# Kernel tuning notes

Measured on AMD Instinct MI355X. Metric: run time of the kernel, lower is better.

Reference implementation:

```python
import jax, jax.numpy as jnp
import numpy as np

N = 50000      # nodes
E = 500000     # edges
R = 4          # num_relations
B = 512        # num graphs in batch
IN = 64        # in_embd
DIN = 6 * IN   # concat of 6 embeddings
H = 256        # layer_embd
O = 256        # out_embd
CARD = [33, 5, 3, 4, 2, 3]


def setup_inputs() -> dict:
    key = jax.random.key(0)
    ks = jax.random.split(key, 24)
    cols = [jax.random.randint(ks[i], (N,), 0, CARD[i], dtype=jnp.int32) for i in range(6)]
    x = jnp.stack(cols, axis=1)                                     # [N,6] categorical atom features
    edge_index = jax.random.randint(ks[6], (2, E), 0, N, dtype=jnp.int32)
    edge_type = jax.random.randint(ks[7], (E,), 0, R, dtype=jnp.int32)
    batch = jnp.sort(jax.random.randint(ks[8], (N,), 0, B, dtype=jnp.int32))

    def g(k, shape, scale):
        return jax.random.normal(k, shape, jnp.float32) * scale

    inp = dict(x=x, edge_index=edge_index, edge_type=edge_type, batch=batch)
    for i in range(6):
        inp[f"emb{i}"] = g(ks[9 + i], (CARD[i], IN), 1.0)
    inp["W1"] = g(ks[15], (R, DIN, H), 0.05)
    inp["root1"] = g(ks[16], (DIN, H), 0.05)
    inp["b1"] = jnp.zeros((H,), jnp.float32)
    inp["W2"] = g(ks[17], (R, H, O), 0.06)
    inp["root2"] = g(ks[18], (H, O), 0.06)
    inp["b2"] = jnp.zeros((O,), jnp.float32)
    inp["g1_w"] = g(ks[19], (O, O), 0.06)
    inp["g1_b"] = jnp.zeros((O,), jnp.float32)
    inp["bn_g"] = jnp.ones((O,), jnp.float32)
    inp["bn_b"] = jnp.zeros((O,), jnp.float32)
    inp["g2_w"] = g(ks[20], (O, 1), 0.06)
    inp["g2_b"] = jnp.zeros((1,), jnp.float32)
    inp["gl_w"] = g(ks[21], (O, 1), 0.06)
    inp["gl_b"] = jnp.zeros((1,), jnp.float32)
    return inp


def rgcn_conv(h, src, dst, etype, W, root, bias):
    # PyG RGCNConv: out_i = x_i @ root + bias + sum_r mean_{j in N_r(i)} (x_j @ W_r)
    xw = jnp.einsum('nd,rdo->rno', h, W)                 # [R,N,O] relation-transformed nodes
    msg = xw[etype, src]                                  # [E,O] gather per edge
    seg = dst * R + etype                                 # combined (node, relation) segment id
    sums = jax.ops.segment_sum(msg, seg, num_segments=N * R)
    cnt = jax.ops.segment_sum(jnp.ones((msg.shape[0],), h.dtype), seg, num_segments=N * R)
    mean = sums / jnp.maximum(cnt, 1.0)[:, None]          # per-relation mean aggregation
    agg = mean.reshape(N, R, -1).sum(axis=1)              # sum over relations
    return agg + h @ root + bias


def reference(x, edge_index, edge_type, batch,
              emb0, emb1, emb2, emb3, emb4, emb5,
              W1, root1, b1, W2, root2, b2,
              g1_w, g1_b, bn_g, bn_b, g2_w, g2_b, gl_w, gl_b):
    embs = [emb0, emb1, emb2, emb3, emb4, emb5]
    feats = jnp.concatenate([embs[i][x[:, i]] for i in range(6)], axis=1)  # [N, 6*IN]
    src, dst = edge_index[0], edge_index[1]
    h = jax.nn.sigmoid(rgcn_conv(feats, src, dst, edge_type, W1, root1, b1))
    h = jax.nn.sigmoid(rgcn_conv(h, src, dst, edge_type, W2, root2, b2))    # [N,O]

    # GlobalAttention gate_nn: Linear -> BatchNorm1d (training-mode stats) -> ReLU -> Linear
    g = h @ g1_w + g1_b
    mu = g.mean(axis=0)
    var = g.var(axis=0)                                   # biased var, as torch BN forward
    g = (g - mu) / jnp.sqrt(var + 1e-5) * bn_g + bn_b
    gate = jax.nn.relu(g) @ g2_w + g2_b                   # [N,1]

    # segment softmax over graphs
    gmax = jax.ops.segment_max(gate, batch, num_segments=B)
    e = jnp.exp(gate - gmax[batch])
    denom = jax.ops.segment_sum(e, batch, num_segments=B)
    attn = e / (denom[batch] + 1e-16)
    pooled = jax.ops.segment_sum(attn * h, batch, num_segments=B)  # [B,O]

    return jax.nn.sigmoid(pooled @ gl_w + gl_b)           # [B,1]
```

## Files before the change

kernel.cpp:

```cpp
#include <hip/hip_runtime.h>
#include <hip/hip_bf16.h>
#include <cstdint>

#define NN 50000
#define NE 500000
#define NR 4
#define NBATCH 512
#define HD 256
#define NSEG (NN*NR)

__constant__ int c_off[6] = {0,33,38,41,45,47};

__device__ __forceinline__ float sigf(float x){ return 1.0f/(1.0f+__expf(-x)); }
__device__ __forceinline__ float bf2f(unsigned short b){ return __uint_as_float((unsigned)b<<16); }
__device__ __forceinline__ unsigned short f2bf(float f){
  unsigned u = __float_as_uint(f);
  return (unsigned short)((u + 0x7fffu + ((u>>16)&1u)) >> 16);
}

typedef short bf16raw8 __attribute__((ext_vector_type(8)));
typedef float f32x4v  __attribute__((ext_vector_type(4)));
union LD16 { uint4 u; bf16raw8 v; };

__global__ void k_weff(const float* __restrict__ e0,const float* __restrict__ e1,
                       const float* __restrict__ e2,const float* __restrict__ e3,
                       const float* __restrict__ e4,const float* __restrict__ e5,
                       const float* __restrict__ W, int rstride,
                       float* __restrict__ out){
  int rc = blockIdx.x, h = threadIdx.x;
  int r = rc/50, cg = rc%50;
  int j, cl;
  if      (cg>=47){j=5;cl=cg-47;} else if (cg>=45){j=4;cl=cg-45;}
  else if (cg>=41){j=3;cl=cg-41;} else if (cg>=38){j=2;cl=cg-38;}
  else if (cg>=33){j=1;cl=cg-33;} else            {j=0;cl=cg;}
  const float* emb = j==0?e0:j==1?e1:j==2?e2:j==3?e3:j==4?e4:e5;
  const float* wb = W + (size_t)r*rstride + (size_t)(j*64)*HD + h;
  float acc = 0.f;
  #pragma unroll 8
  for (int k=0;k<64;k++) acc += emb[cl*64+k]*wb[(size_t)k*HD];
  out[(size_t)rc*HD+h] = acc;
}

__global__ void k_cnt(const int* __restrict__ ei, const int* __restrict__ et,
                      int* __restrict__ cnt){
  int e = blockIdx.x*256 + threadIdx.x;
  if (e >= NE) return;
  atomicAdd(&cnt[ei[NE+e]*NR + et[e]], 1);
}

__global__ void k_b1t(const float* __restrict__ W1eff, const float* __restrict__ R1eff,
                      unsigned short* __restrict__ B1t){
  int id = blockIdx.x*256 + threadIdx.x;
  int k = id & 255, o = id >> 8;
  float v = 0.f;
  if (k < 200) v = W1eff[(size_t)k*HD + o];
  else if (k < 250) v = R1eff[(size_t)(k-200)*HD + o];
  B1t[(size_t)o*256 + k] = f2bf(v);
}

__global__ void k_tconv(const float* __restrict__ W, unsigned short* __restrict__ Wt,
                        int K, int O){
  int id = blockIdx.x*256 + threadIdx.x;
  if (id >= K*O) return;
  int k = id % K, o = id / K;
  Wt[(size_t)o*256 + k] = f2bf(W[(size_t)k*O + o]);
}

#define SC_T 256
#define SC_NB ((NSEG/4 + SC_T - 1)/SC_T)

__global__ void k_scan1(const int* __restrict__ cnt, int* __restrict__ bsum){
  __shared__ int sh[SC_T];
  int b = blockIdx.x, t = threadIdx.x;
  int i4 = b*SC_T + t;
  int s = 0;
  if (i4 < NSEG/4){ int4 v = ((const int4*)cnt)[i4]; s = v.x+v.y+v.z+v.w; }
  sh[t] = s; __syncthreads();
  for (int o=128;o>0;o>>=1){ if (t<o) sh[t]+=sh[t+o]; __syncthreads(); }
  if (t==0) bsum[b] = sh[0];
}

__global__ void k_scan2(const int* __restrict__ bsum, int* __restrict__ boff,
                        int* __restrict__ offs){
  __shared__ int sh[256];
  int t = threadIdx.x;
  int v = (t < SC_NB) ? bsum[t] : 0;
  sh[t] = v; __syncthreads();
  for (int o=1;o<256;o<<=1){
    int add = (t>=o) ? sh[t-o] : 0; __syncthreads();
    sh[t] += add; __syncthreads();
  }
  if (t < SC_NB) boff[t] = sh[t] - v;
  if (t == 255) offs[NSEG] = sh[255];
}

__global__ void k_scan3(const int* __restrict__ cnt, const int* __restrict__ boff,
                        int* __restrict__ offs, int* __restrict__ cursor){
  __shared__ int sh[SC_T];
  int b = blockIdx.x, t = threadIdx.x;
  int i4 = b*SC_T + t;
  int4 v = {0,0,0,0};
  if (i4 < NSEG/4) v = ((const int4*)cnt)[i4];
  int s = v.x+v.y+v.z+v.w;
  sh[t] = s; __syncthreads();
  for (int o=1;o<256;o<<=1){
    int add = (t>=o) ? sh[t-o] : 0; __syncthreads();
    sh[t] += add; __syncthreads();
  }
  if (i4 < NSEG/4){
    int excl = sh[t] - s + boff[b];
    int4 ov; ov.x = excl; ov.y = ov.x+v.x; ov.z = ov.y+v.y; ov.w = ov.z+v.z;
    ((int4*)offs)[i4] = ov; ((int4*)cursor)[i4] = ov;
  }
}

__global__ void k_bin(const int* __restrict__ ei, const int* __restrict__ et,
                      int* __restrict__ cursor, int* __restrict__ esrc){
  int e = blockIdx.x*256 + threadIdx.x;
  if (e >= NE) return;
  int s = ei[e], d = ei[NE+e], t = et[e];
  int slot = atomicAdd(&cursor[d*NR + t], 1);
  esrc[slot] = s;
}

__global__ void k_buildseg(const int* __restrict__ x, const int* __restrict__ offs,
                           const int* __restrict__ esrc, unsigned short* __restrict__ A1){
  int n = blockIdx.x, t = threadIdx.x;
  float v = 0.f;
  if (t < 200){
    int r = t/50, bin = t%50;
    int j, cl;
    if      (bin>=47){j=5;cl=bin-47;} else if (bin>=45){j=4;cl=bin-45;}
    else if (bin>=41){j=3;cl=bin-41;} else if (bin>=38){j=2;cl=bin-38;}
    else if (bin>=33){j=1;cl=bin-33;} else            {j=0;cl=bin;}
    int a = offs[n*NR+r], e2 = offs[n*NR+r+1];
    int c = 0;
    for (int e=a;e<e2;e++){
      int s = esrc[e];
      c += (x[s*6+j] == cl) ? 1 : 0;
    }
    v = (float)c / (float)max(e2-a, 1);
  } else if (t < 250){
    int cg = t - 200;
    #pragma unroll
    for (int j=0;j<6;j++) if (cg == c_off[j] + x[n*6+j]) v = 1.f;
  }
  A1[(size_t)n*256 + t] = f2bf(v);
}

template<bool SIG>
__global__ __launch_bounds__(512) void k_mfma(
    const unsigned short* __restrict__ A,  int lda,
    const unsigned short* __restrict__ Bt,
    const float* __restrict__ bias,
    unsigned short* __restrict__ out0, int ldc0, int n0,
    unsigned short* __restrict__ out1, int ldc1,
    int M){
  constexpr int NK = 8;
  constexpr int K  = 256;
  int tid = threadIdx.x;
  int wave = tid >> 6, lane = tid & 63;
  int wm = (wave >> 1) * 32, wn = (wave & 1) * 64;
  int bm = blockIdx.y * 128, bn = blockIdx.x * 128;
  int lrow = lane & 15, lk8 = (lane >> 4) * 8;

  const unsigned short* aP[2];
  const unsigned short* bP[4];
  #pragma unroll
  for (int mi=0;mi<2;mi++){
    int row = bm + wm + mi*16 + lrow; if (row > M-1) row = M-1;
    aP[mi] = A + (size_t)row*lda + lk8;
  }
  #pragma unroll
  for (int nj=0;nj<4;nj++){
    int col = bn + wn + nj*16 + lrow;
    bP[nj] = Bt + (size_t)col*K + lk8;
  }

  f32x4v acc[2][4] = {};
  bf16raw8 aF[2][2], bF[2][4];

  #pragma unroll
  for (int mi=0;mi<2;mi++){ LD16 t; t.u = *(const uint4*)(aP[mi]); aF[0][mi]=t.v; }
  #pragma unroll
  for (int nj=0;nj<4;nj++){ LD16 t; t.u = *(const uint4*)(bP[nj]); bF[0][nj]=t.v; }

  #pragma unroll
  for (int k=0;k<NK;k++){
    int cur = k & 1, nxt = cur ^ 1;
    if (k+1 < NK){
      #pragma unroll
      for (int mi=0;mi<2;mi++){ LD16 t; t.u = *(const uint4*)(aP[mi] + (k+1)*32); aF[nxt][mi]=t.v; }
      #pragma unroll
      for (int nj=0;nj<4;nj++){ LD16 t; t.u = *(const uint4*)(bP[nj] + (k+1)*32); bF[nxt][nj]=t.v; }
    }
    #pragma unroll
    for (int mi=0;mi<2;mi++)
      #pragma unroll
      for (int nj=0;nj<4;nj++)
        acc[mi][nj] = __builtin_amdgcn_mfma_f32_16x16x32_bf16(aF[cur][mi], bF[cur][nj], acc[mi][nj], 0, 0, 0);
  }

  int r0 = (lane >> 4) * 4;
  #pragma unroll
  for (int mi = 0; mi < 2; mi++){
    #pragma unroll
    for (int i = 0; i < 4; i++){
      int row = bm + wm + mi*16 + r0 + i;
      if (row >= M) continue;
      #pragma unroll
      for (int nj = 0; nj < 4; nj++){
        int col = bn + wn + nj*16 + lrow;
        float v = acc[mi][nj][i];
        if (bias) v += bias[col];
        if (SIG) v = sigf(v);
        if (col < n0) out0[(size_t)row*ldc0 + col] = f2bf(v);
        else          out1[(size_t)row*ldc1 + (col - n0)] = f2bf(v);
      }
    }
  }
}

__global__ void k_comb1(const int* __restrict__ offs, const int* __restrict__ esrc,
                        const unsigned short* __restrict__ zbuf,
                        unsigned short* __restrict__ pacc){
  int gid = blockIdx.x*256 + threadIdx.x;
  int n = gid >> 6;
  if (n >= NN) return;
  int lane = gid & 63;
  float t0=0.f,t1=0.f,t2=0.f,t3=0.f;
  #pragma unroll
  for (int r=0;r<2;r++){
    int a = offs[n*NR+r], b = offs[n*NR+r+1];
    float a0=0.f,a1=0.f,a2=0.f,a3=0.f;
    for (int e=a;e<b;e++){
      int s = esrc[e];
      ushort4 v = *(const ushort4*)(zbuf + (size_t)s*512 + r*256 + lane*4);
      a0+=bf2f(v.x); a1+=bf2f(v.y); a2+=bf2f(v.z); a3+=bf2f(v.w);
    }
    float iv = 1.0f / (float)max(b-a, 1);
    t0+=a0*iv; t1+=a1*iv; t2+=a2*iv; t3+=a3*iv;
  }
  ushort4 o; o.x=f2bf(t0); o.y=f2bf(t1); o.z=f2bf(t2); o.w=f2bf(t3);
  *(ushort4*)(pacc + (size_t)n*HD + lane*4) = o;
}

__global__ void k_comb2(const int* __restrict__ offs, const int* __restrict__ esrc,
                        const unsigned short* __restrict__ zbuf,
                        const unsigned short* __restrict__ pacc,
                        const unsigned short* __restrict__ rootbuf,
                        const float* __restrict__ b2,
                        unsigned short* __restrict__ h2){
  int gid = blockIdx.x*256 + threadIdx.x;
  int n = gid >> 6;
  if (n >= NN) return;
  int lane = gid & 63;
  float t0=0.f,t1=0.f,t2=0.f,t3=0.f;
  #pragma unroll
  for (int r=0;r<2;r++){
    int a = offs[n*NR+2+r], b = offs[n*NR+2+r+1];
    float a0=0.f,a1=0.f,a2=0.f,a3=0.f;
    for (int e=a;e<b;e++){
      int s = esrc[e];
      ushort4 v = *(const ushort4*)(zbuf + (size_t)s*512 + r*256 + lane*4);
      a0+=bf2f(v.x); a1+=bf2f(v.y); a2+=bf2f(v.z); a3+=bf2f(v.w);
    }
    float iv = 1.0f / (float)max(b-a, 1);
    t0+=a0*iv; t1+=a1*iv; t2+=a2*iv; t3+=a3*iv;
  }
  ushort4 p = *(const ushort4*)(pacc + (size_t)n*HD + lane*4);
  ushort4 rt= *(const ushort4*)(rootbuf + (size_t)n*HD + lane*4);
  float4 bb = *(const float4*)(b2 + lane*4);
  ushort4 o;
  o.x = f2bf(sigf(t0 + bf2f(p.x) + bf2f(rt.x) + bb.x));
  o.y = f2bf(sigf(t1 + bf2f(p.y) + bf2f(rt.y) + bb.y));
  o.z = f2bf(sigf(t2 + bf2f(p.z) + bf2f(rt.z) + bb.z));
  o.w = f2bf(sigf(t3 + bf2f(p.w) + bf2f(rt.w) + bb.w));
  *(ushort4*)(h2 + (size_t)n*HD + lane*4) = o;
}

__global__ void k_bnstats(const unsigned short* __restrict__ g, float* __restrict__ chan){
  int c = threadIdx.x;
  int r0 = blockIdx.x*128;
  int rend = min(r0+128, NN);
  float s=0.f, q=0.f;
  for (int row=r0; row<rend; row++){
    float v = bf2f(g[(size_t)row*HD + c]);
    s += v; q += v*v;
  }
  atomicAdd(&chan[c], s); atomicAdd(&chan[HD+c], q);
}

__global__ void k_bnfin(const float* __restrict__ chan, const float* __restrict__ bng,
                        const float* __restrict__ bnb, float* __restrict__ bnp){
  int c = threadIdx.x;
  float mu = chan[c]/(float)NN;
  float var = chan[HD+c]/(float)NN - mu*mu;
  float scale = bng[c]*rsqrtf(var + 1e-5f);
  bnp[c] = bnb[c] - mu*scale;
  bnp[HD+c] = scale;
}

__global__ void k_gate(const unsigned short* __restrict__ g, const float* __restrict__ bnp,
                       const float* __restrict__ g2w, const float* __restrict__ g2b,
                       float* __restrict__ gate){
  int lane = threadIdx.x & 63;
  int n = blockIdx.x*4 + (threadIdx.x>>6);
  if (n >= NN) return;
  float s = 0.f;
  #pragma unroll
  for (int k=0;k<4;k++){
    int c = lane + k*64;
    float v = bf2f(g[(size_t)n*HD + c])*bnp[HD+c] + bnp[c];
    v = fmaxf(v, 0.f);
    s += v * g2w[c];
  }
  #pragma unroll
  for (int o=32;o>0;o>>=1) s += __shfl_down(s, o);
  if (lane==0) gate[n] = s + g2b[0];
}

__global__ void k_goffs(const int* __restrict__ batch, int* __restrict__ goffs){
  int n = blockIdx.x*256 + threadIdx.x;
  if (n >= NN) return;
  int b = batch[n];
  int prev = (n == 0) ? -1 : batch[n-1];
  for (int gg = prev+1; gg <= b; gg++) goffs[gg] = n;
  if (n == NN-1){ for (int gg = b+1; gg <= NBATCH; gg++) goffs[gg] = NN; }
}

__global__ __launch_bounds__(256) void k_poolg(
    const unsigned short* __restrict__ h2, const float* __restrict__ gate,
    const int* __restrict__ goffs, const float* __restrict__ glw,
    const float* __restrict__ glb, float* __restrict__ out){
  __shared__ float red[256];
  int b = blockIdx.x, tid = threadIdx.x;
  int a = goffs[b], e = goffs[b+1];

  float m = -3.4e38f;
  for (int n = a + tid; n < e; n += 256) m = fmaxf(m, gate[n]);
  red[tid] = m; __syncthreads();
  for (int o = 128; o > 0; o >>= 1){ if (tid < o) red[tid] = fmaxf(red[tid], red[tid+o]); __syncthreads(); }
  m = red[0]; __syncthreads();

  float s = 0.f;
  for (int n = a + tid; n < e; n += 256) s += __expf(gate[n] - m);
  red[tid] = s; __syncthreads();
  for (int o = 128; o > 0; o >>= 1){ if (tid < o) red[tid] += red[tid+o]; __syncthreads(); }
  float denom = red[0] + 1e-16f; __syncthreads();

  float acc = 0.f;
  #pragma unroll 4
  for (int n = a; n < e; n++){
    float ev = __expf(gate[n] - m);
    acc += ev * bf2f(h2[(size_t)n*HD + tid]);
  }
  acc /= denom;

  red[tid] = acc * glw[tid]; __syncthreads();
  for (int o = 128; o > 0; o >>= 1){ if (tid < o) red[tid] += red[tid+o]; __syncthreads(); }
  if (tid == 0) out[b] = sigf(red[0] + glb[0]);
}

extern "C" void kernel_launch(void* const* d_in, const int* in_sizes, int n_in,
                              void* d_out, int out_size, void* d_ws, size_t ws_size,
                              hipStream_t stream) {
  const int* x     = (const int*)d_in[0];
  const int* ei    = (const int*)d_in[1];
  const int* et    = (const int*)d_in[2];
  const int* batch = (const int*)d_in[3];
  const float* emb0 = (const float*)d_in[4];
  const float* emb1 = (const float*)d_in[5];
  const float* emb2 = (const float*)d_in[6];
  const float* emb3 = (const float*)d_in[7];
  const float* emb4 = (const float*)d_in[8];
  const float* emb5 = (const float*)d_in[9];
  const float* W1    = (const float*)d_in[10];
  const float* root1 = (const float*)d_in[11];
  const float* b1    = (const float*)d_in[12];
  const float* W2    = (const float*)d_in[13];
  const float* root2 = (const float*)d_in[14];
  const float* b2    = (const float*)d_in[15];
  const float* g1w   = (const float*)d_in[16];
  const float* g1b   = (const float*)d_in[17];
  const float* bng   = (const float*)d_in[18];
  const float* bnb   = (const float*)d_in[19];
  const float* g2w   = (const float*)d_in[20];
  const float* g2b   = (const float*)d_in[21];
  const float* glw   = (const float*)d_in[22];
  const float* glb   = (const float*)d_in[23];
  float* out = (float*)d_out;

  char* w = (char*)d_ws;
  auto alloc = [&](size_t bytes)->char* {
    char* p = w; w += (bytes + 255) & ~(size_t)255; return p;
  };
  char* slotA = alloc((size_t)NN*HD*2);
  unsigned short* A1      = (unsigned short*)slotA;
  unsigned short* rootbuf = (unsigned short*)slotA;
  unsigned short* g       = (unsigned short*)slotA;
  unsigned short* h1 = (unsigned short*)alloc((size_t)NN*HD*2);
  unsigned short* h2 = h1;
  unsigned short* zbuf = (unsigned short*)alloc((size_t)NN*512*2);
  unsigned short* pacc = (unsigned short*)alloc((size_t)NN*HD*2);
  int*   cnt  = (int*)alloc((size_t)NSEG*sizeof(int));
  int*   cursor = cnt;
  int*   offs = (int*)alloc((size_t)(NSEG+1)*sizeof(int));
  int*   bsum = (int*)alloc((size_t)SC_NB*sizeof(int));
  int*   boff = (int*)alloc((size_t)SC_NB*sizeof(int));
  int*   esrc = (int*)alloc((size_t)NE*sizeof(int));
  float* W1eff= (float*)alloc((size_t)200*HD*sizeof(float));
  float* R1eff= (float*)alloc((size_t)50*HD*sizeof(float));
  unsigned short* B1t  = (unsigned short*)alloc((size_t)256*256*2);
  unsigned short* Btz1 = (unsigned short*)alloc((size_t)768*256*2);
  unsigned short* Btz2 = (unsigned short*)alloc((size_t)512*256*2);
  unsigned short* g1wt = (unsigned short*)alloc((size_t)256*256*2);
  float* gate = (float*)alloc((size_t)NN*sizeof(float));
  int*   goffs= (int*)alloc((size_t)(NBATCH+1)*sizeof(int));
  float* chan = (float*)alloc((size_t)2*HD*sizeof(float));
  float* bnp  = (float*)alloc((size_t)2*HD*sizeof(float));

  hipMemsetAsync(cnt,  0, (size_t)NSEG*sizeof(int), stream);
  hipMemsetAsync(chan, 0, (size_t)2*HD*sizeof(float), stream);

  k_weff<<<NR*50, HD, 0, stream>>>(emb0,emb1,emb2,emb3,emb4,emb5, W1, 384*HD, W1eff);
  k_weff<<<50,    HD, 0, stream>>>(emb0,emb1,emb2,emb3,emb4,emb5, root1, 0, R1eff);
  k_b1t<<<256, 256, 0, stream>>>(W1eff, R1eff, B1t);
  k_tconv<<<256, 256, 0, stream>>>(W2,               Btz1,           256, 256);
  k_tconv<<<256, 256, 0, stream>>>(W2 + 256*256,     Btz1 + 256*256, 256, 256);
  k_tconv<<<256, 256, 0, stream>>>(root2,            Btz1 + 512*256, 256, 256);
  k_tconv<<<256, 256, 0, stream>>>(W2 + 2*256*256,   Btz2,           256, 256);
  k_tconv<<<256, 256, 0, stream>>>(W2 + 3*256*256,   Btz2 + 256*256, 256, 256);
  k_tconv<<<256, 256, 0, stream>>>(g1w,              g1wt,           256, 256);

  k_cnt<<<(NE+255)/256, 256, 0, stream>>>(ei, et, cnt);
  k_scan1<<<SC_NB, SC_T, 0, stream>>>(cnt, bsum);
  k_scan2<<<1, 256, 0, stream>>>(bsum, boff, offs);
  k_scan3<<<SC_NB, SC_T, 0, stream>>>(cnt, boff, offs, cursor);
  k_bin<<<(NE+255)/256, 256, 0, stream>>>(ei, et, cursor, esrc);

  k_buildseg<<<NN, 256, 0, stream>>>(x, offs, esrc, A1);

  k_goffs<<<(NN+255)/256, 256, 0, stream>>>(batch, goffs);

  dim3 g256(2, (NN+127)/128);
  k_mfma<true><<<g256, 512, 0, stream>>>(A1, 256, B1t, b1, h1, 256, 256, nullptr, 0, NN);

  dim3 g768(6, (NN+127)/128);
  k_mfma<false><<<g768, 512, 0, stream>>>(h1, 256, Btz1, nullptr, zbuf, 512, 512, rootbuf, 256, NN);
  k_comb1<<<(NN*64+255)/256, 256, 0, stream>>>(offs, esrc, zbuf, pacc);

  dim3 g512(4, (NN+127)/128);
  k_mfma<false><<<g512, 512, 0, stream>>>(h1, 256, Btz2, nullptr, zbuf, 512, 512, nullptr, 0, NN);
  k_comb2<<<(NN*64+255)/256, 256, 0, stream>>>(offs, esrc, zbuf, pacc, rootbuf, b2, h2);

  k_mfma<false><<<g256, 512, 0, stream>>>(h2, 256, g1wt, g1b, g, 256, 256, nullptr, 0, NN);
  k_bnstats<<<(NN+127)/128, HD, 0, stream>>>(g, chan);
  k_bnfin<<<1, HD, 0, stream>>>(chan, bng, bnb, bnp);

  k_gate<<<(NN+3)/4, 256, 0, stream>>>(g, bnp, g2w, g2b, gate);
  k_poolg<<<NBATCH, 256, 0, stream>>>(h2, gate, goffs, glw, glb, out);
}
```

Measured before the change: 688.3 us.

## Stage GEMM tiles through swizzled LDS with double buffering and coalesced stores

```diff
diff --git a/kernel.cpp b/kernel.cpp
--- a/kernel.cpp
+++ b/kernel.cpp
@@ -149,75 +149,109 @@
 }
 
 template<bool SIG>
-__global__ __launch_bounds__(512) void k_mfma(
+__global__ __launch_bounds__(256) void k_mfma(
     const unsigned short* __restrict__ A,  int lda,
     const unsigned short* __restrict__ Bt,
     const float* __restrict__ bias,
     unsigned short* __restrict__ out0, int ldc0, int n0,
     unsigned short* __restrict__ out1, int ldc1,
     int M){
-  constexpr int NK = 8;
-  constexpr int K  = 256;
+  constexpr int NT = 4;
+  __shared__ unsigned short lds[2][2][128*64];
   int tid = threadIdx.x;
   int wave = tid >> 6, lane = tid & 63;
-  int wm = (wave >> 1) * 32, wn = (wave & 1) * 64;
+  int wm = (wave >> 1) * 64, wn = (wave & 1) * 64;
   int bm = blockIdx.y * 128, bn = blockIdx.x * 128;
-  int lrow = lane & 15, lk8 = (lane >> 4) * 8;
-
-  const unsigned short* aP[2];
-  const unsigned short* bP[4];
-  #pragma unroll
-  for (int mi=0;mi<2;mi++){
-    int row = bm + wm + mi*16 + lrow; if (row > M-1) row = M-1;
-    aP[mi] = A + (size_t)row*lda + lk8;
-  }
-  #pragma unroll
-  for (int nj=0;nj<4;nj++){
-    int col = bn + wn + nj*16 + lrow;
-    bP[nj] = Bt + (size_t)col*K + lk8;
-  }
-
-  f32x4v acc[2][4] = {};
-  bf16raw8 aF[2][2], bF[2][4];
-
-  #pragma unroll
-  for (int mi=0;mi<2;mi++){ LD16 t; t.u = *(const uint4*)(aP[mi]); aF[0][mi]=t.v; }
-  #pragma unroll
-  for (int nj=0;nj<4;nj++){ LD16 t; t.u = *(const uint4*)(bP[nj]); bF[0][nj]=t.v; }
-
-  #pragma unroll
-  for (int k=0;k<NK;k++){
-    int cur = k & 1, nxt = cur ^ 1;
-    if (k+1 < NK){
+  int lrow = lane & 15, q = lane >> 4;
+
+  uint4 rA[4], rB[4];
+
+  auto load_regs = [&](int kt){
+    #pragma unroll
+    for (int v=0; v<4; v++){
+      int c = v*256 + tid;
+      int row = c >> 3, kc = c & 7;
+      int ra = bm + row; if (ra > M-1) ra = M-1;
+      rA[v] = *(const uint4*)(A  + (size_t)ra*lda + kt*64 + kc*8);
+      int cb = bn + row;
+      rB[v] = *(const uint4*)(Bt + (size_t)cb*256 + kt*64 + kc*8);
+    }
+  };
+  auto write_lds = [&](int buf){
+    #pragma unroll
+    for (int v=0; v<4; v++){
+      int c = v*256 + tid;
+      int row = c >> 3, kc = c & 7;
+      int pc = kc ^ (row & 7);
+      *(uint4*)&lds[buf][0][row*64 + pc*8] = rA[v];
+      *(uint4*)&lds[buf][1][row*64 + pc*8] = rB[v];
+    }
+  };
+
+  f32x4v acc[4][4] = {};
+
+  load_regs(0); write_lds(0);
+  __syncthreads();
+
+  for (int kt=0; kt<NT; ++kt){
+    int cur = kt & 1;
+    bool pf = (kt+1 < NT);
+    if (pf) load_regs(kt+1);
+    #pragma unroll
+    for (int s=0; s<2; s++){
+      bf16raw8 aF[4], bF[4];
       #pragma unroll
-      for (int mi=0;mi<2;mi++){ LD16 t; t.u = *(const uint4*)(aP[mi] + (k+1)*32); aF[nxt][mi]=t.v; }
+      for (int mi=0; mi<4; mi++){
+        int row = wm + mi*16 + lrow;
+        int pc = (s*4 + q) ^ (row & 7);
+        LD16 t; t.u = *(const uint4*)&lds[cur][0][row*64 + pc*8];
+        aF[mi] = t.v;
+      }
       #pragma unroll
-      for (int nj=0;nj<4;nj++){ LD16 t; t.u = *(const uint4*)(bP[nj] + (k+1)*32); bF[nxt][nj]=t.v; }
-    }
+      for (int nj=0; nj<4; nj++){
+        int col = wn + nj*16 + lrow;
+        int pc = (s*4 + q) ^ (col & 7);
+        LD16 t; t.u = *(const uint4*)&lds[cur][1][col*64 + pc*8];
+        bF[nj] = t.v;
+      }
+      #pragma unroll
+      for (int mi=0; mi<4; mi++)
+        #pragma unroll
+        for (int nj=0; nj<4; nj++)
+          acc[mi][nj] = __builtin_amdgcn_mfma_f32_16x16x32_bf16(aF[mi], bF[nj], acc[mi][nj], 0, 0, 0);
+    }
+    if (pf) write_lds(cur ^ 1);
+    __syncthreads();
+  }
+
+  unsigned short* cst = &lds[0][0][0];
+  int r0 = q * 4;
+  #pragma unroll
+  for (int mi=0; mi<4; mi++){
     #pragma unroll
-    for (int mi=0;mi<2;mi++)
+    for (int i=0; i<4; i++){
+      int row = wm + mi*16 + r0 + i;
       #pragma unroll
-      for (int nj=0;nj<4;nj++)
-        acc[mi][nj] = __builtin_amdgcn_mfma_f32_16x16x32_bf16(aF[cur][mi], bF[cur][nj], acc[mi][nj], 0, 0, 0);
-  }
-
-  int r0 = (lane >> 4) * 4;
-  #pragma unroll
-  for (int mi = 0; mi < 2; mi++){
-    #pragma unroll
-    for (int i = 0; i < 4; i++){
-      int row = bm + wm + mi*16 + r0 + i;
-      if (row >= M) continue;
-      #pragma unroll
-      for (int nj = 0; nj < 4; nj++){
-        int col = bn + wn + nj*16 + lrow;
+      for (int nj=0; nj<4; nj++){
+        int col = wn + nj*16 + lrow;
         float v = acc[mi][nj][i];
-        if (bias) v += bias[col];
-        if (SIG) v = sigf(v);
-        if (col < n0) out0[(size_t)row*ldc0 + col] = f2bf(v);
-        else          out1[(size_t)row*ldc1 + (col - n0)] = f2bf(v);
+        if (bias) v += bias[bn + col];
+        if (SIG)  v = sigf(v);
+        cst[row*128 + col] = f2bf(v);
       }
     }
+  }
+  __syncthreads();
+  #pragma unroll
+  for (int v=0; v<8; v++){
+    int p = v*256 + tid;
+    int row = p >> 4, cc = p & 15;
+    int rg = bm + row;
+    if (rg >= M) continue;
+    uint4 val = *(const uint4*)&cst[row*128 + cc*8];
+    int cg = bn + cc*8;
+    if (cg < n0) *(uint4*)(out0 + (size_t)rg*ldc0 + cg)        = val;
+    else         *(uint4*)(out1 + (size_t)rg*ldc1 + (cg - n0)) = val;
   }
 }
 
@@ -444,17 +478,17 @@
   k_goffs<<<(NN+255)/256, 256, 0, stream>>>(batch, goffs);
 
   dim3 g256(2, (NN+127)/128);
-  k_mfma<true><<<g256, 512, 0, stream>>>(A1, 256, B1t, b1, h1, 256, 256, nullptr, 0, NN);
+  k_mfma<true><<<g256, 256, 0, stream>>>(A1, 256, B1t, b1, h1, 256, 256, nullptr, 0, NN);
 
   dim3 g768(6, (NN+127)/128);
-  k_mfma<false><<<g768, 512, 0, stream>>>(h1, 256, Btz1, nullptr, zbuf, 512, 512, rootbuf, 256, NN);
+  k_mfma<false><<<g768, 256, 0, stream>>>(h1, 256, Btz1, nullptr, zbuf, 512, 512, rootbuf, 256, NN);
   k_comb1<<<(NN*64+255)/256, 256, 0, stream>>>(offs, esrc, zbuf, pacc);
 
   dim3 g512(4, (NN+127)/128);
-  k_mfma<false><<<g512, 512, 0, stream>>>(h1, 256, Btz2, nullptr, zbuf, 512, 512, nullptr, 0, NN);
+  k_mfma<false><<<g512, 256, 0, stream>>>(h1, 256, Btz2, nullptr, zbuf, 512, 512, nullptr, 0, NN);
   k_comb2<<<(NN*64+255)/256, 256, 0, stream>>>(offs, esrc, zbuf, pacc, rootbuf, b2, h2);
 
-  k_mfma<false><<<g256, 512, 0, stream>>>(h2, 256, g1wt, g1b, g, 256, 256, nullptr, 0, NN);
+  k_mfma<false><<<g256, 256, 0, stream>>>(h2, 256, g1wt, g1b, g, 256, 256, nullptr, 0, NN);
   k_bnstats<<<(NN+127)/128, HD, 0, stream>>>(g, chan);
   k_bnfin<<<1, HD, 0, stream>>>(chan, bng, bnb, bnp);
 
```

New measurement: 658.1 us. 4.4% less time.
